# Optimization experiments

Measured on AMD Instinct MI355X. Metric: run time of the kernel, lower is better.

Reference implementation:

```python
import jax, jax.numpy as jnp
import numpy as np

NUM_LAYERS = 3


def setup_inputs() -> dict:
    key = jax.random.key(0)
    ks = jax.random.split(key, 12)
    N, E, D_IN, D, ED = 50000, 800000, 6, 64, 4
    return {
        "x": jax.random.normal(ks[0], (N, D_IN), dtype=jnp.float32),
        "edge_index": jax.random.randint(ks[1], (2, E), 0, N, dtype=jnp.int64),
        "edge_attr": jax.random.normal(ks[2], (E, ED), dtype=jnp.float32),
        "z_soft": jax.random.uniform(ks[3], (E, ED), dtype=jnp.float32),
        "W_nt": jax.random.normal(ks[4], (D, D_IN), dtype=jnp.float32) * 0.1,
        "b_nt": jax.random.normal(ks[5], (D,), dtype=jnp.float32) * 0.1,
        "weight": jax.random.normal(ks[6], (NUM_LAYERS, D, D), dtype=jnp.float32) * 0.1,
        "W_ih": jax.random.normal(ks[7], (3 * D, D), dtype=jnp.float32) * 0.1,
        "W_hh": jax.random.normal(ks[8], (3 * D, D), dtype=jnp.float32) * 0.1,
        "b_ih": jax.random.normal(ks[9], (3 * D,), dtype=jnp.float32) * 0.1,
        "b_hh": jax.random.normal(ks[10], (3 * D,), dtype=jnp.float32) * 0.1,
    }


def gru_cell(m, h, W_ih, W_hh, b_ih, b_hh):
    # PyTorch GRUCell: gates ordered (r, z, n)
    gi = m @ W_ih.T + b_ih
    gh = h @ W_hh.T + b_hh
    i_r, i_z, i_n = jnp.split(gi, 3, axis=-1)
    h_r, h_z, h_n = jnp.split(gh, 3, axis=-1)
    r = jax.nn.sigmoid(i_r + h_r)
    z = jax.nn.sigmoid(i_z + h_z)
    n = jnp.tanh(i_n + r * h_n)
    return (1.0 - z) * n + z * h


def reference(x, edge_index, edge_attr, z_soft, W_nt, b_nt, weight, W_ih, W_hh, b_ih, b_hh):
    # node_transform: Linear + ReLU
    h = jax.nn.relu(x @ W_nt.T + b_nt)  # [N, D]
    # edge_attr gating (faithful to source; unused since edge_weight=None)
    _ = z_soft * edge_attr
    src, dst = edge_index[0], edge_index[1]
    N = h.shape[0]
    for i in range(NUM_LAYERS):
        m = h @ weight[i]                                   # [N, D]
        agg = jax.ops.segment_sum(m[src], dst, num_segments=N)  # gather-scatter add
        h = gru_cell(agg, h, W_ih, W_hh, b_ih, b_hh)
    return h
```

## Files before the change

kernel.cpp:

```cpp
#include <hip/hip_runtime.h>
#include <hip/hip_bf16.h>
#include <stdint.h>

#define D 64
typedef __hip_bfloat16 bf16;
typedef unsigned short u16;
typedef __attribute__((ext_vector_type(8))) short bf16x8;
typedef __attribute__((ext_vector_type(4))) float f32x4;

__device__ __forceinline__ float bf2f(u16 u) { return __uint_as_float(((uint32_t)u) << 16); }
__device__ __forceinline__ u16 f2bf(float f) { return __bfloat16_as_ushort(__float2bfloat16(f)); }

template <bool F32>
__device__ __forceinline__ float ld(const void* p, int i) {
    if constexpr (F32) return ((const float*)p)[i];
    else return bf2f(((const u16*)p)[i]);
}

__global__ __launch_bounds__(256) void detect_kernel(const void* x, const int* ei, int* flags) {
    __shared__ float smax[256];
    __shared__ int sor[256];
    int t = threadIdx.x;
    const u16* xs = (const u16*)x;
    float mx = 0.f;
#pragma unroll
    for (int i = 0; i < 16; ++i) {
        float a = fabsf(bf2f(xs[t * 16 + i]));
        if (!(a == a)) a = 1e30f;
        mx = fmaxf(mx, a);
    }
    int any = 0;
#pragma unroll
    for (int i = 0; i < 8; ++i) any |= ei[2 * (t * 8 + i) + 1];
    smax[t] = mx; sor[t] = any;
    __syncthreads();
    for (int s = 128; s > 0; s >>= 1) {
        if (t < s) { smax[t] = fmaxf(smax[t], smax[t + s]); sor[t] |= sor[t + s]; }
        __syncthreads();
    }
    if (t == 0) { flags[0] = (smax[0] > 1000.f) ? 1 : 0; flags[1] = (sor[0] != 0) ? 1 : 0; }
}

__global__ __launch_bounds__(256) void convert_edges(const int* __restrict__ flags,
                                                     const int* __restrict__ ei,
                                                     uint32_t* __restrict__ pe, int E, int N) {
    int i0 = blockIdx.x * 1024 + threadIdx.x;
    bool i32 = flags[1] != 0;
#pragma unroll
    for (int u = 0; u < 4; ++u) {
        int i = i0 + u * 256;
        if (i < E) {
            int src, dst;
            if (i32) { src = ei[i];     dst = ei[E + i]; }
            else     { src = ei[2 * i]; dst = ei[2 * (E + i)]; }
            uint32_t v;
            if ((unsigned)src >= (unsigned)N || (unsigned)dst >= (unsigned)N) v = 0xFFFFFFFFu;
            else v = (uint32_t)(u16)src | ((uint32_t)dst << 16);
            pe[i] = v;
        }
    }
}

#define N_WCT 36864
#define N_WTH 12288
#define N_B   384
template <bool F32>
__device__ __forceinline__ void nt_body(const void* x, const void* Wnt, const void* bnt,
                                        u16* ht, int N, int blk) {
    int gid = blk * 256 + threadIdx.x;
    if (gid >= N * D) return;
    int n = gid >> 6, c = gid & 63;
    float acc = ld<F32>(bnt, c);
#pragma unroll
    for (int k = 0; k < 6; ++k)
        acc = fmaf(ld<F32>(x, n * 6 + k), ld<F32>(Wnt, c * 6 + k), acc);
    ht[gid] = f2bf(fmaxf(acc, 0.f));
}
template <bool F32>
__device__ __forceinline__ void wc_body(const void* W, const void* Wih, const void* Whh,
                                        const void* bih, const void* bhh,
                                        u16* WCh, u16* WCl, u16* WVh, u16* WVl,
                                        float* B, int blk) {
    int i = blk * 256 + threadIdx.x;
    if (i < N_WCT) {
        int l = i / 12288, rem = i % 12288, k = rem / 192, r = rem % 192;
        float acc = 0.f;
#pragma unroll 8
        for (int j = 0; j < 64; ++j)
            acc = fmaf(ld<F32>(W, l * 4096 + k * 64 + j), ld<F32>(Wih, r * 64 + j), acc);
        u16 hi = f2bf(acc);
        WCh[l * 12288 + r * 64 + k] = hi;
        WCl[l * 12288 + r * 64 + k] = f2bf(acc - bf2f(hi));
    } else if (i < N_WCT + N_WTH) {
        int rem = i - N_WCT;
        int k = rem / 192, r = rem % 192;
        float v = ld<F32>(Whh, r * 64 + k);
        u16 hi = f2bf(v);
        WVh[r * 64 + k] = hi;
        WVl[r * 64 + k] = f2bf(v - bf2f(hi));
    } else if (i < N_WCT + N_WTH + N_B) {
        int rem = i - N_WCT - N_WTH;
        B[rem] = (rem < 192) ? ld<F32>(bih, rem) : ld<F32>(bhh, rem - 192);
    }
}
__global__ __launch_bounds__(256) void prep_all(const int* __restrict__ flags,
                                                const void* x, const void* Wnt, const void* bnt,
                                                const void* W, const void* Wih, const void* Whh,
                                                const void* bih, const void* bhh,
                                                u16* ht, u16* WCh, u16* WCl, u16* WVh, u16* WVl,
                                                float* B,
                                                const uint32_t* __restrict__ pe,
                                                int* __restrict__ cnt,
                                                u16* __restrict__ ss16, int* __restrict__ novf,
                                                int* __restrict__ ovf,
                                                int E, int N, int NT_BLK, int WC_BLK, int EPS) {
    int b = blockIdx.x;
    if (b < NT_BLK) {
        if (flags[0]) nt_body<true>(x, Wnt, bnt, ht, N, b);
        else          nt_body<false>(x, Wnt, bnt, ht, N, b);
    } else if (b < NT_BLK + WC_BLK) {
        if (flags[0]) wc_body<true>(W, Wih, Whh, bih, bhh, WCh, WCl, WVh, WVl, B, b - NT_BLK);
        else          wc_body<false>(W, Wih, Whh, bih, bhh, WCh, WCl, WVh, WVl, B, b - NT_BLK);
    } else {
        int bf = b - NT_BLK - WC_BLK;
        unsigned shard = (unsigned)(b & 7);
        int beg = (bf >> 3) * EPS;
        int end = beg + EPS; if (end > E) end = E;
        for (int i = beg + (int)threadIdx.x; i < end; i += 256) {
            uint32_t e = pe[i];
            int dst = (int)(e >> 16);
            if ((((unsigned)dst >> 4) & 7u) != shard) continue;
            if (dst >= N) continue;
            int src = (int)(e & 0xffffu);
            int pos = atomicAdd(&cnt[dst], 1);
            if (pos < 64) ss16[(size_t)dst * 64 + pos] = (u16)src;
            else {
                int o = atomicAdd(novf, 1);
                if (o < E) { ovf[2 * o] = dst; ovf[2 * o + 1] = src; }
            }
        }
    }
}

#define NPB 16
#define LSTR 68

#define GLOAD(A, P, J) \
    _Pragma("unroll") for (int q = 0; q < 16; ++q) { \
        int ix_ = __shfl(iv[P], (J) + q); \
        bool vq_ = ((J) + q) < dg[P]; \
        ix_ = vq_ ? ix_ : 0; \
        float tv_ = bf2f(ht[(size_t)ix_ * D + lane]); \
        A[q] = vq_ ? tv_ : 0.f; }
#define GSUM(A) (((((A)[0]+(A)[1])+((A)[2]+(A)[3]))+(((A)[4]+(A)[5])+((A)[6]+(A)[7]))) \
               + ((((A)[8]+(A)[9])+((A)[10]+(A)[11]))+(((A)[12]+(A)[13])+((A)[14]+(A)[15]))))

__global__ __launch_bounds__(256, 3) void layer_fused(const int* __restrict__ flags,
                                                   const u16* __restrict__ ht,
                                                   const int* __restrict__ cnt,
                                                   const u16* __restrict__ ss16,
                                                   const int* __restrict__ novf,
                                                   const int* __restrict__ ovf,
                                                   const u16* __restrict__ WCh,
                                                   const u16* __restrict__ WCl,
                                                   const u16* __restrict__ WVh,
                                                   const u16* __restrict__ WVl,
                                                   const float* __restrict__ B,
                                                   u16* __restrict__ houtb,
                                                   void* __restrict__ dout,
                                                   int N) {
    __shared__ alignas(16) float LA[NPB * LSTR];
    __shared__ alignas(16) float LH[NPB * LSTR];
    __shared__ alignas(16) u16 Ahi[NPB * 64];
    __shared__ alignas(16) u16 Alo[NPB * 64];
    __shared__ alignas(16) u16 Hb[NPB * 64];
    int t = threadIdx.x;
    int n0 = blockIdx.x * NPB;
    int lane = t & 63;
    int w = t >> 6;
    int w4 = w * 4;

    {
        if (t < 128) {
            int row = t >> 3, c = (t & 7) * 8;
            bool v = (n0 + row) < N;
            uint4 vh = make_uint4(0u, 0u, 0u, 0u);
            if (v) vh = *(const uint4*)(ht + (size_t)(n0 + row) * D + c);
            float4 f0, f1;
            f0.x = bf2f((u16)(vh.x & 0xffff)); f0.y = bf2f((u16)(vh.x >> 16));
            f0.z = bf2f((u16)(vh.y & 0xffff)); f0.w = bf2f((u16)(vh.y >> 16));
            f1.x = bf2f((u16)(vh.z & 0xffff)); f1.y = bf2f((u16)(vh.z >> 16));
            f1.z = bf2f((u16)(vh.w & 0xffff)); f1.w = bf2f((u16)(vh.w >> 16));
            *(float4*)&LH[row * LSTR + c]     = f0;
            *(float4*)&LH[row * LSTR + c + 4] = f1;
            *(uint4*)((char*)Hb + row * 128 + ((c * 2) ^ ((row & 7) << 4))) = vh;
        }
    }

    int dg[4]; int iv[4];
#pragma unroll
    for (int p = 0; p < 4; ++p) {
        int n = n0 + w4 + p;
        dg[p] = 0; iv[p] = 0;
        if (n < N) {
            int c = cnt[n]; dg[p] = (c > 64) ? 64 : c;
            iv[p] = (int)ss16[(size_t)n * 64 + lane];
        }
    }
    float acc0, acc1, acc2, acc3;
    {
        float a0[16], a1[16], a2[16], a3[16];
        GLOAD(a0, 0, 0) GLOAD(a1, 1, 0) GLOAD(a2, 2, 0) GLOAD(a3, 3, 0)
        acc0 = GSUM(a0); acc1 = GSUM(a1); acc2 = GSUM(a2); acc3 = GSUM(a3);
    }
#define GTAIL(P, ACC) if (dg[P] > 16) { \
        float b_[16]; \
        GLOAD(b_, P, 16) \
        ACC += GSUM(b_); \
        for (int j = 32; j < dg[P]; ++j) \
            ACC += bf2f(ht[(size_t)__shfl(iv[P], j) * D + lane]); }
    GTAIL(0, acc0) GTAIL(1, acc1) GTAIL(2, acc2) GTAIL(3, acc3)
    LA[(w4 + 0) * LSTR + lane] = acc0;
    LA[(w4 + 1) * LSTR + lane] = acc1;
    LA[(w4 + 2) * LSTR + lane] = acc2;
    LA[(w4 + 3) * LSTR + lane] = acc3;
    __syncthreads();
    {
        int nv = novf[0];
        if (nv > 0) {
            if (nv > (1 << 20)) nv = (1 << 20);
            for (int o = w; o < nv; o += 4) {
                int dst = ovf[2 * o];
                if (dst >= n0 && dst < n0 + NPB) {
                    int src = ovf[2 * o + 1];
                    atomicAdd(&LA[(dst - n0) * LSTR + lane], bf2f(ht[(size_t)src * D + lane]));
                }
            }
        }
    }
    __syncthreads();
    {
        int row = t >> 4, c = (t & 15) * 4;
        float4 v = *(const float4*)&LA[row * LSTR + c];
        u16 h0 = f2bf(v.x), h1 = f2bf(v.y), h2 = f2bf(v.z), h3 = f2bf(v.w);
        uint2 hh, llv;
        hh.x = (uint32_t)h0 | ((uint32_t)h1 << 16);
        hh.y = (uint32_t)h2 | ((uint32_t)h3 << 16);
        llv.x = (uint32_t)f2bf(v.x - bf2f(h0)) | ((uint32_t)f2bf(v.y - bf2f(h1)) << 16);
        llv.y = (uint32_t)f2bf(v.z - bf2f(h2)) | ((uint32_t)f2bf(v.w - bf2f(h3)) << 16);
        int off = row * 128 + ((c * 2) ^ ((row & 7) << 4));
        *(uint2*)((char*)Ahi + off) = hh;
        *(uint2*)((char*)Alo + off) = llv;
    }
    __syncthreads();

    int r = lane & 15, g = lane >> 4;
    int aoff0 = r * 128 + (((g * 16) + 0) ^ ((r & 7) << 4));
    int aoff1 = r * 128 + (((g * 16) + 64) ^ ((r & 7) << 4));
    bf16x8 aH0 = *(const bf16x8*)((const char*)Ahi + aoff0);
    bf16x8 aH1 = *(const bf16x8*)((const char*)Ahi + aoff1);
    bf16x8 aL0 = *(const bf16x8*)((const char*)Alo + aoff0);
    bf16x8 aL1 = *(const bf16x8*)((const char*)Alo + aoff1);
    bf16x8 hB0 = *(const bf16x8*)((const char*)Hb + aoff0);
    bf16x8 hB1 = *(const bf16x8*)((const char*)Hb + aoff1);

#define WFRAG(P, nt, ks) (*(const bf16x8*)((const char*)(P) + ((nt) * 16 + r) * 128 + (ks) * 64 + g * 16))
#define DO_TILE(nt, ai, ah) { \
    bf16x8 wch0 = WFRAG(WCh, nt, 0), wch1 = WFRAG(WCh, nt, 1); \
    bf16x8 wcl0 = WFRAG(WCl, nt, 0), wcl1 = WFRAG(WCl, nt, 1); \
    bf16x8 wvh0 = WFRAG(WVh, nt, 0), wvh1 = WFRAG(WVh, nt, 1); \
    bf16x8 wvl0 = WFRAG(WVl, nt, 0), wvl1 = WFRAG(WVl, nt, 1); \
    ai = __builtin_amdgcn_mfma_f32_16x16x32_bf16(aH0, wch0, ai, 0, 0, 0); \
    ai = __builtin_amdgcn_mfma_f32_16x16x32_bf16(aH1, wch1, ai, 0, 0, 0); \
    ai = __builtin_amdgcn_mfma_f32_16x16x32_bf16(aL0, wch0, ai, 0, 0, 0); \
    ai = __builtin_amdgcn_mfma_f32_16x16x32_bf16(aL1, wch1, ai, 0, 0, 0); \
    ai = __builtin_amdgcn_mfma_f32_16x16x32_bf16(aH0, wcl0, ai, 0, 0, 0); \
    ai = __builtin_amdgcn_mfma_f32_16x16x32_bf16(aH1, wcl1, ai, 0, 0, 0); \
    ah = __builtin_amdgcn_mfma_f32_16x16x32_bf16(hB0, wvh0, ah, 0, 0, 0); \
    ah = __builtin_amdgcn_mfma_f32_16x16x32_bf16(hB1, wvh1, ah, 0, 0, 0); \
    ah = __builtin_amdgcn_mfma_f32_16x16x32_bf16(hB0, wvl0, ah, 0, 0, 0); \
    ah = __builtin_amdgcn_mfma_f32_16x16x32_bf16(hB1, wvl1, ah, 0, 0, 0); }

    f32x4 air = {0.f, 0.f, 0.f, 0.f}, aiz = air, ain = air;
    f32x4 ahr = air, ahz = air, ahn = air;
    DO_TILE(w, air, ahr);
    DO_TILE(w + 4, aiz, ahz);
    DO_TILE(w + 8, ain, ahn);

    {
        int ch = w * 16 + r;
        float br = B[ch] + B[192 + ch];
        float bz = B[64 + ch] + B[256 + ch];
        float bi = B[128 + ch];
        float bh = B[320 + ch];
        int nb = g * 4;
#pragma unroll
        for (int j = 0; j < 4; ++j) {
            float gr = air[j] + ahr[j] + br;
            float gz = aiz[j] + ahz[j] + bz;
            float rr = 1.f / (1.f + __expf(-gr));
            float zz = 1.f / (1.f + __expf(-gz));
            float nx = ain[j] + bi + rr * (ahn[j] + bh);
            float th = 1.f - 2.f / (1.f + __expf(2.f * nx));
            float hold = LH[(nb + j) * LSTR + ch];
            LA[(nb + j) * LSTR + ch] = (1.f - zz) * th + zz * hold;
        }
    }
    __syncthreads();
    if (t < 128) {
        int row = t >> 3, c = (t & 7) * 8;
        int n = n0 + row;
        if (n < N) {
            float4 v0 = *(const float4*)&LA[row * LSTR + c];
            float4 v1 = *(const float4*)&LA[row * LSTR + c + 4];
            size_t idx = (size_t)n * D + c;
            if (houtb || !flags[0]) {
                uint4 o;
                o.x = (uint32_t)f2bf(v0.x) | ((uint32_t)f2bf(v0.y) << 16);
                o.y = (uint32_t)f2bf(v0.z) | ((uint32_t)f2bf(v0.w) << 16);
                o.z = (uint32_t)f2bf(v1.x) | ((uint32_t)f2bf(v1.y) << 16);
                o.w = (uint32_t)f2bf(v1.z) | ((uint32_t)f2bf(v1.w) << 16);
                if (houtb) *(uint4*)(houtb + idx) = o;
                else       *(uint4*)((u16*)dout + idx) = o;
            } else {
                *(float4*)((float*)dout + idx)     = v0;
                *(float4*)((float*)dout + idx + 4) = v1;
            }
        }
    }
}

extern "C" void kernel_launch(void* const* d_in, const int* in_sizes, int n_in,
                              void* d_out, int out_size, void* d_ws, size_t ws_size,
                              hipStream_t stream) {
    const void* x   = d_in[0];
    const int*  ei  = (const int*)d_in[1];
    const void* Wnt = d_in[4];
    const void* bnt = d_in[5];
    const void* Wt  = d_in[6];
    const void* Wih = d_in[7];
    const void* Whh = d_in[8];
    const void* bih = d_in[9];
    const void* bhh = d_in[10];

    int N = in_sizes[0] / 6;
    int E = in_sizes[1] / 2;
    int ND = N * D;

    int* flags = (int*)d_ws;
    float* B   = (float*)((char*)d_ws + 256);
    u16* WCh = (u16*)(B + N_B);
    u16* WCl = WCh + N_WCT;
    u16* WVh = WCl + N_WCT;
    u16* WVl = WVh + N_WTH;
    u16* htA = WVl + N_WTH;
    u16* htB = htA + ND;
    int* cnt  = (int*)(htB + ND);
    int* novf = cnt + N;
    u16* ss16 = (u16*)(novf + 1);
    int* ovf  = (int*)(ss16 + (size_t)N * 64);
    uint32_t* pe = (uint32_t*)(ovf + 2 * (size_t)E);

    int NT_BLK = (ND + 255) / 256;
    int WC_BLK = (N_WCT + N_WTH + N_B + 255) / 256;
    int FS = (E + 1023) / 1024;
    int EPS = (E + FS - 1) / FS;
    int FI_BLK = 8 * FS;
    int CV_BLK = (E + 1023) / 1024;

    hipMemsetAsync(cnt, 0, (size_t)(N + 1) * sizeof(int), stream);
    detect_kernel<<<1, 256, 0, stream>>>(x, ei, flags);
    convert_edges<<<CV_BLK, 256, 0, stream>>>(flags, ei, pe, E, N);
    prep_all<<<NT_BLK + WC_BLK + FI_BLK, 256, 0, stream>>>(flags, x, Wnt, bnt, Wt, Wih, Whh,
                                                           bih, bhh, htA, WCh, WCl, WVh, WVl, B,
                                                           pe, cnt, ss16, novf, ovf,
                                                           E, N, NT_BLK, WC_BLK, EPS);

    u16* hcur = htA;
    u16* hnxt = htB;
    for (int layer = 0; layer < 3; ++layer) {
        bool last = (layer == 2);
        layer_fused<<<(N + NPB - 1) / NPB, 256, 0, stream>>>(flags, hcur, cnt, ss16, novf, ovf,
                                                             WCh + layer * 12288, WCl + layer * 12288,
                                                             WVh, WVl, B,
                                                             last ? nullptr : hnxt,
                                                             last ? d_out : nullptr, N);
        u16* t = hcur; hcur = hnxt; hnxt = t;
    }
}
```

Before: 313.4 us.

## Split layer into plane-partitioned gather kernel and separate GRU gates kernel

Stores node features as two 32-column planes so each gather block touches only a 3.2MB half of the feature table, improving L2 locality. Aggregation moves into a separate high-occupancy gather kernel that reads 4 neighbours per load with packed bf16 pairs and writes hi/lo split aggregates to global memory. The GRU gates kernel then consumes those aggregates. This adds an extra launch and a global round-trip of the aggregates per layer. The overflow buffer is capped, and overflow edges are now scanned serially by every block.

```diff
diff --git a/kernel.cpp b/kernel.cpp
--- a/kernel.cpp
+++ b/kernel.cpp
@@ -7,6 +7,8 @@
 typedef unsigned short u16;
 typedef __attribute__((ext_vector_type(8))) short bf16x8;
 typedef __attribute__((ext_vector_type(4))) float f32x4;
+
+#define OVF_CAP 65536
 
 __device__ __forceinline__ float bf2f(u16 u) { return __uint_as_float(((uint32_t)u) << 16); }
 __device__ __forceinline__ u16 f2bf(float f) { return __bfloat16_as_ushort(__float2bfloat16(f)); }
@@ -74,7 +76,8 @@
 #pragma unroll
     for (int k = 0; k < 6; ++k)
         acc = fmaf(ld<F32>(x, n * 6 + k), ld<F32>(Wnt, c * 6 + k), acc);
-    ht[gid] = f2bf(fmaxf(acc, 0.f));
+    size_t off = (size_t)(c >> 5) * (size_t)N * 32 + (size_t)n * 32 + (c & 31);
+    ht[off] = f2bf(fmaxf(acc, 0.f));
 }
 template <bool F32>
 __device__ __forceinline__ void wc_body(const void* W, const void* Wih, const void* Whh,
@@ -136,39 +139,111 @@
             if (pos < 64) ss16[(size_t)dst * 64 + pos] = (u16)src;
             else {
                 int o = atomicAdd(novf, 1);
-                if (o < E) { ovf[2 * o] = dst; ovf[2 * o + 1] = src; }
+                if (o < OVF_CAP) { ovf[2 * o] = dst; ovf[2 * o + 1] = src; }
             }
         }
+    }
+}
+
+__global__ __launch_bounds__(256, 8) void gather_kernel(const u16* __restrict__ htp,
+                                                        const int* __restrict__ cnt,
+                                                        const u16* __restrict__ ss16,
+                                                        const int* __restrict__ novf,
+                                                        const int* __restrict__ ovf,
+                                                        uint32_t* __restrict__ AhiP,
+                                                        uint32_t* __restrict__ AloP,
+                                                        int N, int NTILES) {
+    int b = blockIdx.x;
+    int g = b >> 3, r = b & 7;
+    int plane = r >> 2;
+    int tile = g * 4 + (r & 3);
+    if (tile >= NTILES) return;
+    int n0 = tile * 16;
+    int t = threadIdx.x;
+    int lane = t & 63;
+    int w4 = (t >> 6) * 4;
+    int q = lane >> 4, dcol = lane & 15;
+    const uint32_t* hp = (const uint32_t*)htp + (size_t)plane * N * 16;
+
+    int dg[4]; int iv[4];
+#pragma unroll
+    for (int p = 0; p < 4; ++p) {
+        int n = n0 + w4 + p;
+        dg[p] = 0; iv[p] = 0;
+        if (n < N) {
+            int c = __builtin_nontemporal_load(cnt + n);
+            dg[p] = (c > 64) ? 64 : c;
+            iv[p] = (int)__builtin_nontemporal_load(ss16 + (size_t)n * 64 + lane);
+        }
+    }
+    float e0[4] = {0.f, 0.f, 0.f, 0.f}, e1[4] = {0.f, 0.f, 0.f, 0.f};
+#define GP(P, JB, NIT) \
+    _Pragma("unroll") for (int it_ = 0; it_ < (NIT); ++it_) { \
+        int j_ = (JB) + it_ * 4 + q; \
+        int ix_ = __shfl(iv[P], j_); \
+        bool v_ = j_ < dg[P]; \
+        uint32_t d_ = hp[(uint32_t)(v_ ? ix_ : 0) * 16u + (uint32_t)dcol]; \
+        d_ = v_ ? d_ : 0u; \
+        e0[P] += __uint_as_float(d_ << 16); \
+        e1[P] += __uint_as_float(d_ & 0xffff0000u); }
+    GP(0, 0, 4) GP(1, 0, 4) GP(2, 0, 4) GP(3, 0, 4)
+    if (dg[0] > 16) GP(0, 16, 4)
+    if (dg[1] > 16) GP(1, 16, 4)
+    if (dg[2] > 16) GP(2, 16, 4)
+    if (dg[3] > 16) GP(3, 16, 4)
+    if (dg[0] > 32) GP(0, 32, 8)
+    if (dg[1] > 32) GP(1, 32, 8)
+    if (dg[2] > 32) GP(2, 32, 8)
+    if (dg[3] > 32) GP(3, 32, 8)
+#pragma unroll
+    for (int p = 0; p < 4; ++p) {
+        e0[p] += __shfl_xor(e0[p], 16); e0[p] += __shfl_xor(e0[p], 32);
+        e1[p] += __shfl_xor(e1[p], 16); e1[p] += __shfl_xor(e1[p], 32);
+    }
+    {
+        int nv = novf[0];
+        if (nv > 0) {
+            if (nv > OVF_CAP) nv = OVF_CAP;
+            for (int o = 0; o < nv; ++o) {
+                int dst = ovf[2 * o];
+#pragma unroll
+                for (int p = 0; p < 4; ++p) {
+                    if (dst == n0 + w4 + p) {
+                        uint32_t d_ = hp[(uint32_t)ovf[2 * o + 1] * 16u + (uint32_t)dcol];
+                        e0[p] += __uint_as_float(d_ << 16);
+                        e1[p] += __uint_as_float(d_ & 0xffff0000u);
+                    }
+                }
+            }
+        }
+    }
+#pragma unroll
+    for (int p = 0; p < 4; ++p) {
+        int n = n0 + w4 + p;
+        if (n >= N) continue;
+        u16 h0 = f2bf(e0[p]), h1 = f2bf(e1[p]);
+        uint32_t hid = (uint32_t)h0 | ((uint32_t)h1 << 16);
+        uint32_t lod = (uint32_t)f2bf(e0[p] - bf2f(h0)) | ((uint32_t)f2bf(e1[p] - bf2f(h1)) << 16);
+        size_t off = (size_t)plane * N * 16 + (size_t)n * 16 + (size_t)dcol;
+        if (q == 0) AhiP[off] = hid;
+        else if (q == 1) AloP[off] = lod;
     }
 }
 
 #define NPB 16
 #define LSTR 68
-
-#define GLOAD(A, P, J) \
-    _Pragma("unroll") for (int q = 0; q < 16; ++q) { \
-        int ix_ = __shfl(iv[P], (J) + q); \
-        bool vq_ = ((J) + q) < dg[P]; \
-        ix_ = vq_ ? ix_ : 0; \
-        float tv_ = bf2f(ht[(size_t)ix_ * D + lane]); \
-        A[q] = vq_ ? tv_ : 0.f; }
-#define GSUM(A) (((((A)[0]+(A)[1])+((A)[2]+(A)[3]))+(((A)[4]+(A)[5])+((A)[6]+(A)[7]))) \
-               + ((((A)[8]+(A)[9])+((A)[10]+(A)[11]))+(((A)[12]+(A)[13])+((A)[14]+(A)[15]))))
-
-__global__ __launch_bounds__(256, 3) void layer_fused(const int* __restrict__ flags,
-                                                   const u16* __restrict__ ht,
-                                                   const int* __restrict__ cnt,
-                                                   const u16* __restrict__ ss16,
-                                                   const int* __restrict__ novf,
-                                                   const int* __restrict__ ovf,
-                                                   const u16* __restrict__ WCh,
-                                                   const u16* __restrict__ WCl,
-                                                   const u16* __restrict__ WVh,
-                                                   const u16* __restrict__ WVl,
-                                                   const float* __restrict__ B,
-                                                   u16* __restrict__ houtb,
-                                                   void* __restrict__ dout,
-                                                   int N) {
+__global__ __launch_bounds__(256, 3) void gates_kernel(const int* __restrict__ flags,
+                                                       const u16* __restrict__ htp,
+                                                       const uint32_t* __restrict__ AhiP,
+                                                       const uint32_t* __restrict__ AloP,
+                                                       const u16* __restrict__ WCh,
+                                                       const u16* __restrict__ WCl,
+                                                       const u16* __restrict__ WVh,
+                                                       const u16* __restrict__ WVl,
+                                                       const float* __restrict__ B,
+                                                       u16* __restrict__ houtp,
+                                                       void* __restrict__ dout,
+                                                       int N) {
     __shared__ alignas(16) float LA[NPB * LSTR];
     __shared__ alignas(16) float LH[NPB * LSTR];
     __shared__ alignas(16) u16 Ahi[NPB * 64];
@@ -178,79 +253,34 @@
     int n0 = blockIdx.x * NPB;
     int lane = t & 63;
     int w = t >> 6;
-    int w4 = w * 4;
-
-    {
-        if (t < 128) {
-            int row = t >> 3, c = (t & 7) * 8;
-            bool v = (n0 + row) < N;
-            uint4 vh = make_uint4(0u, 0u, 0u, 0u);
-            if (v) vh = *(const uint4*)(ht + (size_t)(n0 + row) * D + c);
-            float4 f0, f1;
-            f0.x = bf2f((u16)(vh.x & 0xffff)); f0.y = bf2f((u16)(vh.x >> 16));
-            f0.z = bf2f((u16)(vh.y & 0xffff)); f0.w = bf2f((u16)(vh.y >> 16));
-            f1.x = bf2f((u16)(vh.z & 0xffff)); f1.y = bf2f((u16)(vh.z >> 16));
-            f1.z = bf2f((u16)(vh.w & 0xffff)); f1.w = bf2f((u16)(vh.w >> 16));
-            *(float4*)&LH[row * LSTR + c]     = f0;
-            *(float4*)&LH[row * LSTR + c + 4] = f1;
-            *(uint4*)((char*)Hb + row * 128 + ((c * 2) ^ ((row & 7) << 4))) = vh;
-        }
-    }
-
-    int dg[4]; int iv[4];
-#pragma unroll
-    for (int p = 0; p < 4; ++p) {
-        int n = n0 + w4 + p;
-        dg[p] = 0; iv[p] = 0;
+
+    if (t < 128) {
+        int row = t >> 3, c = (t & 7) * 8;
+        int n = n0 + row;
+        uint4 vh = make_uint4(0u, 0u, 0u, 0u);
+        if (n < N)
+            vh = *(const uint4*)(htp + (size_t)(c >> 5) * N * 32 + (size_t)n * 32 + (c & 31));
+        float4 f0, f1;
+        f0.x = bf2f((u16)(vh.x & 0xffff)); f0.y = bf2f((u16)(vh.x >> 16));
+        f0.z = bf2f((u16)(vh.y & 0xffff)); f0.w = bf2f((u16)(vh.y >> 16));
+        f1.x = bf2f((u16)(vh.z & 0xffff)); f1.y = bf2f((u16)(vh.z >> 16));
+        f1.z = bf2f((u16)(vh.w & 0xffff)); f1.w = bf2f((u16)(vh.w >> 16));
+        *(float4*)&LH[row * LSTR + c]     = f0;
+        *(float4*)&LH[row * LSTR + c + 4] = f1;
+        *(uint4*)((char*)Hb + row * 128 + ((c * 2) ^ ((row & 7) << 4))) = vh;
+    } else {
+        int t2 = t - 128;
+        int row = t2 >> 3, c = (t2 & 7) * 8;
+        int n = n0 + row;
+        uint4 vh = make_uint4(0u, 0u, 0u, 0u), vl = make_uint4(0u, 0u, 0u, 0u);
         if (n < N) {
-            int c = cnt[n]; dg[p] = (c > 64) ? 64 : c;
-            iv[p] = (int)ss16[(size_t)n * 64 + lane];
-        }
-    }
-    float acc0, acc1, acc2, acc3;
-    {
-        float a0[16], a1[16], a2[16], a3[16];
-        GLOAD(a0, 0, 0) GLOAD(a1, 1, 0) GLOAD(a2, 2, 0) GLOAD(a3, 3, 0)
-        acc0 = GSUM(a0); acc1 = GSUM(a1); acc2 = GSUM(a2); acc3 = GSUM(a3);
-    }
-#define GTAIL(P, ACC) if (dg[P] > 16) { \
-        float b_[16]; \
-        GLOAD(b_, P, 16) \
-        ACC += GSUM(b_); \
-        for (int j = 32; j < dg[P]; ++j) \
-            ACC += bf2f(ht[(size_t)__shfl(iv[P], j) * D + lane]); }
-    GTAIL(0, acc0) GTAIL(1, acc1) GTAIL(2, acc2) GTAIL(3, acc3)
-    LA[(w4 + 0) * LSTR + lane] = acc0;
-    LA[(w4 + 1) * LSTR + lane] = acc1;
-    LA[(w4 + 2) * LSTR + lane] = acc2;
-    LA[(w4 + 3) * LSTR + lane] = acc3;
-    __syncthreads();
-    {
-        int nv = novf[0];
-        if (nv > 0) {
-            if (nv > (1 << 20)) nv = (1 << 20);
-            for (int o = w; o < nv; o += 4) {
-                int dst = ovf[2 * o];
-                if (dst >= n0 && dst < n0 + NPB) {
-                    int src = ovf[2 * o + 1];
-                    atomicAdd(&LA[(dst - n0) * LSTR + lane], bf2f(ht[(size_t)src * D + lane]));
-                }
-            }
-        }
-    }
-    __syncthreads();
-    {
-        int row = t >> 4, c = (t & 15) * 4;
-        float4 v = *(const float4*)&LA[row * LSTR + c];
-        u16 h0 = f2bf(v.x), h1 = f2bf(v.y), h2 = f2bf(v.z), h3 = f2bf(v.w);
-        uint2 hh, llv;
-        hh.x = (uint32_t)h0 | ((uint32_t)h1 << 16);
-        hh.y = (uint32_t)h2 | ((uint32_t)h3 << 16);
-        llv.x = (uint32_t)f2bf(v.x - bf2f(h0)) | ((uint32_t)f2bf(v.y - bf2f(h1)) << 16);
-        llv.y = (uint32_t)f2bf(v.z - bf2f(h2)) | ((uint32_t)f2bf(v.w - bf2f(h3)) << 16);
+            size_t o = (size_t)(c >> 5) * N * 16 + (size_t)n * 16 + ((c & 31) >> 1);
+            vh = *(const uint4*)(AhiP + o);
+            vl = *(const uint4*)(AloP + o);
+        }
         int off = row * 128 + ((c * 2) ^ ((row & 7) << 4));
-        *(uint2*)((char*)Ahi + off) = hh;
-        *(uint2*)((char*)Alo + off) = llv;
+        *(uint4*)((char*)Ahi + off) = vh;
+        *(uint4*)((char*)Alo + off) = vl;
     }
     __syncthreads();
 
@@ -313,18 +343,19 @@
         if (n < N) {
             float4 v0 = *(const float4*)&LA[row * LSTR + c];
             float4 v1 = *(const float4*)&LA[row * LSTR + c + 4];
-            size_t idx = (size_t)n * D + c;
-            if (houtb || !flags[0]) {
+            if (houtp || !flags[0]) {
                 uint4 o;
                 o.x = (uint32_t)f2bf(v0.x) | ((uint32_t)f2bf(v0.y) << 16);
                 o.y = (uint32_t)f2bf(v0.z) | ((uint32_t)f2bf(v0.w) << 16);
                 o.z = (uint32_t)f2bf(v1.x) | ((uint32_t)f2bf(v1.y) << 16);
                 o.w = (uint32_t)f2bf(v1.z) | ((uint32_t)f2bf(v1.w) << 16);
-                if (houtb) *(uint4*)(houtb + idx) = o;
-                else       *(uint4*)((u16*)dout + idx) = o;
+                if (houtp)
+                    *(uint4*)(houtp + (size_t)(c >> 5) * N * 32 + (size_t)n * 32 + (c & 31)) = o;
+                else
+                    *(uint4*)((u16*)dout + (size_t)n * D + c) = o;
             } else {
-                *(float4*)((float*)dout + idx)     = v0;
-                *(float4*)((float*)dout + idx + 4) = v1;
+                *(float4*)((float*)dout + (size_t)n * D + c)     = v0;
+                *(float4*)((float*)dout + (size_t)n * D + c + 4) = v1;
             }
         }
     }
@@ -355,11 +386,13 @@
     u16* WVl = WVh + N_WTH;
     u16* htA = WVl + N_WTH;
     u16* htB = htA + ND;
-    int* cnt  = (int*)(htB + ND);
+    uint32_t* AhiP = (uint32_t*)(htB + ND);
+    uint32_t* AloP = AhiP + (size_t)N * 32;
+    int* cnt  = (int*)(AloP + (size_t)N * 32);
     int* novf = cnt + N;
     u16* ss16 = (u16*)(novf + 1);
     int* ovf  = (int*)(ss16 + (size_t)N * 64);
-    uint32_t* pe = (uint32_t*)(ovf + 2 * (size_t)E);
+    uint32_t* pe = (uint32_t*)(ovf + 2 * (size_t)OVF_CAP);
 
     int NT_BLK = (ND + 255) / 256;
     int WC_BLK = (N_WCT + N_WTH + N_B + 255) / 256;
@@ -367,6 +400,8 @@
     int EPS = (E + FS - 1) / FS;
     int FI_BLK = 8 * FS;
     int CV_BLK = (E + 1023) / 1024;
+    int NTILES = (N + NPB - 1) / NPB;
+    int GA_BLK = ((NTILES + 3) / 4) * 8;
 
     hipMemsetAsync(cnt, 0, (size_t)(N + 1) * sizeof(int), stream);
     detect_kernel<<<1, 256, 0, stream>>>(x, ei, flags);
@@ -380,11 +415,13 @@
     u16* hnxt = htB;
     for (int layer = 0; layer < 3; ++layer) {
         bool last = (layer == 2);
-        layer_fused<<<(N + NPB - 1) / NPB, 256, 0, stream>>>(flags, hcur, cnt, ss16, novf, ovf,
-                                                             WCh + layer * 12288, WCl + layer * 12288,
-                                                             WVh, WVl, B,
-                                                             last ? nullptr : hnxt,
-                                                             last ? d_out : nullptr, N);
+        gather_kernel<<<GA_BLK, 256, 0, stream>>>(hcur, cnt, ss16, novf, ovf,
+                                                  AhiP, AloP, N, NTILES);
+        gates_kernel<<<NTILES, 256, 0, stream>>>(flags, hcur, AhiP, AloP,
+                                                 WCh + layer * 12288, WCl + layer * 12288,
+                                                 WVh, WVl, B,
+                                                 last ? nullptr : hnxt,
+                                                 last ? d_out : nullptr, N);
         u16* t = hcur; hcur = hnxt; hnxt = t;
     }
 }
```

Result: slower. 344.5 us (+9.9%).
